# Optimization experiments

Hardware: AMD Instinct MI355X
Metric: run time of the kernel (lower is better)

## Reference

```python
import jax, jax.numpy as jnp
import numpy as np

IN_DIM = 5
HIDDEN = 256
NUM_LAYERS = 2
OUT_DIM = 3
B, T = 256, 512


def setup_inputs() -> dict:
    key = jax.random.key(0)
    ks = jax.random.split(key, 16)
    s = 1.0 / np.sqrt(HIDDEN)  # PyTorch LSTM init scale
    inp = {
        "x": jax.random.normal(ks[0], (B, T, IN_DIM), dtype=jnp.float32),
        # layer 0 (input dim 5)
        "Wih0": jax.random.uniform(ks[1], (4 * HIDDEN, IN_DIM), minval=-s, maxval=s),
        "Whh0": jax.random.uniform(ks[2], (4 * HIDDEN, HIDDEN), minval=-s, maxval=s),
        "bih0": jax.random.uniform(ks[3], (4 * HIDDEN,), minval=-s, maxval=s),
        "bhh0": jax.random.uniform(ks[4], (4 * HIDDEN,), minval=-s, maxval=s),
        # layer 1 (input dim HIDDEN)
        "Wih1": jax.random.uniform(ks[5], (4 * HIDDEN, HIDDEN), minval=-s, maxval=s),
        "Whh1": jax.random.uniform(ks[6], (4 * HIDDEN, HIDDEN), minval=-s, maxval=s),
        "bih1": jax.random.uniform(ks[7], (4 * HIDDEN,), minval=-s, maxval=s),
        "bhh1": jax.random.uniform(ks[8], (4 * HIDDEN,), minval=-s, maxval=s),
        # head: Linear(HIDDEN, 3)
        "Wh": jax.random.uniform(ks[9], (OUT_DIM, HIDDEN), minval=-s, maxval=s),
        "bh": jax.random.uniform(ks[10], (OUT_DIM,), minval=-s, maxval=s),
    }
    return inp


def _lstm_layer(x, Wih, Whh, bih, bhh):
    # x: [B, T, D_in] -> h_seq: [B, T, H]
    Bn, Tn, _ = x.shape
    H = Whh.shape[1]
    # precompute input contribution for all timesteps: [T, B, 4H]
    pre = jnp.einsum("btd,gd->tbg", x, Wih) + bih + bhh

    def step(carry, gates_in):
        h, c = carry
        gates = gates_in + h @ Whh.T  # [B, 4H]
        i, f, g, o = jnp.split(gates, 4, axis=-1)  # PyTorch gate order
        i = jax.nn.sigmoid(i)
        f = jax.nn.sigmoid(f)
        g = jnp.tanh(g)
        o = jax.nn.sigmoid(o)
        c = f * c + i * g
        h = o * jnp.tanh(c)
        return (h, c), h

    h0 = jnp.zeros((Bn, H), dtype=x.dtype)
    c0 = jnp.zeros((Bn, H), dtype=x.dtype)
    _, h_seq = jax.lax.scan(step, (h0, c0), pre)  # h_seq: [T, B, H]
    return jnp.transpose(h_seq, (1, 0, 2))  # [B, T, H]


def reference(x, Wih0, Whh0, bih0, bhh0, Wih1, Whh1, bih1, bhh1, Wh, bh):
    h = _lstm_layer(x, Wih0, Whh0, bih0, bhh0)
    h = _lstm_layer(h, Wih1, Whh1, bih1, bhh1)
    # head applied pointwise; only the last timestep is kept, so apply to last step
    last = h[:, -1, :]  # [B, H]
    y = jax.nn.sigmoid(jax.nn.relu(last) @ Wh.T + bh)  # [B, 3]
    return y[:, None, :]  # [B, 1, 3]
```

## Files before the change

### kernel.cpp

```cpp
#include <hip/hip_runtime.h>
#include <hip/hip_bf16.h>

typedef unsigned short u16;
typedef signed char i8;
typedef __attribute__((ext_vector_type(4))) float f32x4;
typedef __attribute__((ext_vector_type(4))) int i32x4;
typedef __attribute__((ext_vector_type(8))) short bf16x8;
typedef __attribute__((ext_vector_type(2))) unsigned int u32x2;

#define HID 256
#define NG 1024
#define TSTEPS 512
#define BATCH 256
#define CH 16
#define NCH 32
#define BB 4
#define HSTR 288
#define LOG2E 1.4426950408889634f
#define PRE_TSTR 262144
#define H0C_TSTR 65536

#define GB0 128
#define GB1 160
#define NBLK 224

#define MFMA_BF16(a, b, c) __builtin_amdgcn_mfma_f32_16x16x32_bf16((a), (b), (c), 0, 0, 0)
#define MFMA_I8(a, b, c)   __builtin_amdgcn_mfma_i32_16x16x64_i8((a), (b), (c), 0, 0, 0)

__device__ __forceinline__ float rcpf_(float x) {
#if __has_builtin(__builtin_amdgcn_rcpf)
    return __builtin_amdgcn_rcpf(x);
#else
    return 1.f / x;
#endif
}
__device__ __forceinline__ float exp2_(float x) {
#if __has_builtin(__builtin_amdgcn_exp2f)
    return __builtin_amdgcn_exp2f(x);
#else
    return exp2f(x);
#endif
}
__device__ __forceinline__ float sigm2(float y) { return rcpf_(1.f + exp2_(-y)); }
__device__ __forceinline__ float tanh2(float y2) { return fmaf(-2.f, rcpf_(exp2_(y2) + 1.f), 1.f); }
__device__ __forceinline__ u16 f2bf(float v){ __hip_bfloat16 h=__float2bfloat16(v); return __builtin_bit_cast(u16,h); }
__device__ __forceinline__ float bf2f(u16 u){ unsigned x=((unsigned)u)<<16; return __builtin_bit_cast(float,x); }

__global__ void prep_a(const float* __restrict__ Whh0, const float* __restrict__ Whh1,
                       const float* __restrict__ bih0, const float* __restrict__ bhh0,
                       const float* __restrict__ bih1, const float* __restrict__ bhh1,
                       float* __restrict__ qs0, float* __restrict__ dq0s,
                       float* __restrict__ qs1, float* __restrict__ dq1s,
                       float* __restrict__ b0s, float* __restrict__ b1s) {
    int r = blockIdx.x * blockDim.x + threadIdx.x;
    if (r >= NG) return;
    float m0 = 1e-20f, m1 = 1e-20f;
    for (int k = 0; k < HID; k++) {
        m0 = fmaxf(m0, fabsf(Whh0[r * HID + k]));
        m1 = fmaxf(m1, fabsf(Whh1[r * HID + k]));
    }
    qs0[r] = 127.f / m0;   dq0s[r] = m0 / 16129.f * LOG2E;
    qs1[r] = 127.f / m1;   dq1s[r] = m1 / 16129.f * LOG2E;
    b0s[r] = (bih0[r] + bhh0[r]) * LOG2E;
    b1s[r] = (bih1[r] + bhh1[r]) * LOG2E;
}

__global__ void prep_b(const float* __restrict__ x,
    const float* __restrict__ Wih0, const float* __restrict__ Whh0,
    const float* __restrict__ Wih1, const float* __restrict__ Whh1,
    const float* __restrict__ qs0, const float* __restrict__ qs1,
    i8* __restrict__ wi80, i8* __restrict__ wi81,
    u16* __restrict__ wih1f, u16* __restrict__ wih0f,
    i8* __restrict__ hs0, i8* __restrict__ hs1,
    float* __restrict__ cs0, float* __restrict__ cs1, u16* __restrict__ xpad)
{
    const int stride = gridDim.x * blockDim.x;
    const int tid = blockIdx.x * blockDim.x + threadIdx.x;
    for (int i = tid; i < NG * HID; i += stride) {
        int e = i & 15, l = (i >> 4) & 63, kc = (i >> 10) & 3, gt = i >> 12;
        int row = 16 * gt + (l & 15);
        int k = kc * 64 + (l >> 4) * 16 + e;
        float q0 = __builtin_rintf(Whh0[row * HID + k] * qs0[row]);
        float q1 = __builtin_rintf(Whh1[row * HID + k] * qs1[row]);
        wi80[i] = (i8)fminf(fmaxf(q0, -127.f), 127.f);
        wi81[i] = (i8)fminf(fmaxf(q1, -127.f), 127.f);
    }
    for (int i = tid; i < NG * HID; i += stride) {
        int gt = i >> 12, kk = (i >> 9) & 7, l = (i >> 3) & 63, e = i & 7;
        wih1f[i] = f2bf(Wih1[(16 * gt + (l & 15)) * HID + kk * 32 + (l >> 4) * 8 + e] * LOG2E);
    }
    for (int i = tid; i < 32768; i += stride) {
        int gt = i >> 9, l = (i >> 3) & 63, e = i & 7;
        int k = (l >> 4) * 8 + e;
        wih0f[i] = (k < 5) ? f2bf(Wih0[(16 * gt + (l & 15)) * 5 + k] * LOG2E) : (u16)0;
    }
    for (int i = tid; i < TSTEPS * BATCH * 8; i += stride) {
        int tok = i >> 3, k = i & 7, t = tok >> 8, b = tok & 255;
        xpad[i] = (k < 5) ? f2bf(x[((size_t)b * TSTEPS + t) * 5 + k]) : (u16)0;
    }
    for (int i = tid; i < BATCH * HID; i += stride) { hs0[i] = 0; hs1[i] = 0; cs0[i] = 0.f; cs1[i] = 0.f; }
}

__global__ __launch_bounds__(1024) __attribute__((amdgpu_waves_per_eu(4, 4)))
void stage_fused(int L,
    const u16* __restrict__ xpad8, const u16* __restrict__ wih0f, const float* __restrict__ b0s,
    const u16* __restrict__ wih1f, const float* __restrict__ b1s,
    u16* __restrict__ p0w, const u16* __restrict__ p0r,
    u16* __restrict__ h0w, const u16* __restrict__ h0r,
    u16* __restrict__ p1w, const u16* __restrict__ p1r,
    const i8* __restrict__ wi80, const i8* __restrict__ wi81,
    const float* __restrict__ dq0s, const float* __restrict__ dq1s,
    i8* __restrict__ hs0, i8* __restrict__ hs1,
    float* __restrict__ cs0, float* __restrict__ cs1)
{
    __shared__ __align__(16) char smem[16384];
    const int bid = blockIdx.x;
    const int tid = threadIdx.x, lane = tid & 63;
    const int col = lane & 15, kgrp = lane >> 4;

    if (bid < GB0) {
        const int layer = bid >> 6;
        if (layer == 0) { if (L < 1 || L > NCH) return; }
        else            { if (L < 3 || L > NCH + 2) return; }
        i8 (*h_lds)[BB * HSTR] = (i8 (*)[BB * HSTR])smem;
        const int btile = bid & 63;
        const u16* pre   = layer ? p1r : p0r;
        const i8*  wi8   = layer ? wi81 : wi80;
        const float* dq  = layer ? dq1s : dq0s;
        i8*    h_state   = layer ? hs1 : hs0;
        float* c_state   = layer ? cs1 : cs0;
        const int w = tid >> 6;
        const int b0 = btile * BB;
        const int u = w * 16 + col;

        float sc[4];
        i32x4 wv[4][4];
#pragma unroll
        for (int j = 0; j < 4; j++) {
            const int gt = 16 * j + w;
            sc[j] = dq[gt * 16 + col];
#pragma unroll
            for (int kc = 0; kc < 4; kc++)
                wv[j][kc] = ((const i32x4*)wi8)[(gt * 4 + kc) * 64 + lane];
        }
        if (tid < 64 * BB) {
            const int rrow = tid >> 6, cc = (tid & 63) * 4;
            *(int*)&h_lds[0][rrow * HSTR + cc] = *(const int*)&h_state[(b0 + rrow) * HID + cc];
        }
        float c_reg = c_state[(size_t)(b0 + kgrp) * HID + u];

        const u16* pb = pre + ((size_t)btile << 12) + (u << 2) + kgrp;
        u16 pvA[4], pvB[4];
#pragma unroll
        for (int j = 0; j < 4; j++) pvA[j] = pb[j << 10];
        const size_t h0base = ((((size_t)(w >> 1) * 16 + (btile >> 2)) * 4
                               + ((w & 1) * 2 + (col >> 3))) * 16
                              + ((btile & 3) * 4 + kgrp)) * 8 + (col & 7);
        __syncthreads();

#define REC_STEP(T, CUR, PVC, PVN) do {                                             \
        _Pragma("unroll")                                                           \
        for (int j = 0; j < 4; j++)                                                 \
            asm volatile("" : "+v"(wv[j][0]), "+v"(wv[j][1]),                       \
                              "+v"(wv[j][2]), "+v"(wv[j][3]));                      \
        i32x4 acc[4];                                                               \
        _Pragma("unroll")                                                           \
        for (int j = 0; j < 4; j++) acc[j] = (i32x4){0, 0, 0, 0};                   \
        _Pragma("unroll")                                                           \
        for (int kc = 0; kc < 4; kc++) {                                            \
            i32x4 a_ = *(const i32x4*)&h_lds[CUR][(col >> 2) * HSTR + kc * 64 + kgrp * 16]; \
            _Pragma("unroll")                                                       \
            for (int j = 0; j < 4; j++) acc[j] = MFMA_I8(a_, wv[j][kc], acc[j]);    \
        }                                                                           \
        const int tn_ = ((T) + 1 < CH) ? (T) + 1 : (T);                             \
        _Pragma("unroll")                                                           \
        for (int j = 0; j < 4; j++) PVN[j] = pb[(size_t)tn_ * PRE_TSTR + (j << 10)];\
        const float yi = fmaf((float)acc[0][0], sc[0], bf2f(PVC[0]));               \
        const float yf = fmaf((float)acc[1][0], sc[1], bf2f(PVC[1]));               \
        const float yg = fmaf((float)acc[2][0], sc[2], bf2f(PVC[2]));               \
        const float yo = fmaf((float)acc[3][0], sc[3], bf2f(PVC[3]));               \
        const float iv = sigm2(yi), fv = sigm2(yf), ov = sigm2(yo);                 \
        const float gv = tanh2(yg + yg);                                            \
        const float cn = fmaf(fv, c_reg, iv * gv);                                  \
        c_reg = cn;                                                                 \
        const float hv = ov * tanh2(cn * (2.f * LOG2E));                            \
        h_lds[(CUR) ^ 1][kgrp * HSTR + u] = (i8)__float2int_rn(hv * 127.f);         \
        if (layer == 0)                                                             \
            h0w[h0base + (size_t)(T) * H0C_TSTR] = f2bf(hv);                        \
        asm volatile("s_waitcnt lgkmcnt(0)" ::: "memory");                          \
        __builtin_amdgcn_s_barrier();                                               \
        __builtin_amdgcn_sched_barrier(0);                                          \
    } while (0)

#pragma unroll 1
        for (int t2 = 0; t2 < CH; t2 += 2) {
            REC_STEP(t2,     0, pvA, pvB);
            REC_STEP(t2 + 1, 1, pvB, pvA);
        }
#undef REC_STEP

        c_state[(size_t)(b0 + kgrp) * HID + u] = c_reg;
        if (tid < 64 * BB) {
            const int rrow = tid >> 6, cc = (tid & 63) * 4;
            *(int*)&h_state[(b0 + rrow) * HID + cc] = *(const int*)&h_lds[0][rrow * HSTR + cc];
        }
        return;
    } else if (bid < GB1) {
        if (L >= NCH) return;
        const int g = bid - GB0;
        const int tp = g >> 1, bh = g & 1;
        const int w = tid >> 6;
        const int j = w >> 2;
        float bias[4];
        bf16x8 wv4[4];
#pragma unroll
        for (int tm = 0; tm < 4; tm++) {
            const int tile = w * 4 + tm;
            bias[tm] = b0s[tile * 16 + col];
            wv4[tm] = *(const bf16x8*)&wih0f[((size_t)tile * 64 + lane) * 8];
        }
        const u16* Ab = xpad8 + ((size_t)L * CH + tp) * BATCH * 8;
#pragma unroll 1
        for (int bt = 0; bt < 8; bt++) {
            const int btg = bh * 8 + bt;
            bf16x8 af = {0, 0, 0, 0, 0, 0, 0, 0};
            if (kgrp == 0) af = *(const bf16x8*)&Ab[(btg * 16 + col) * 8];
            f32x4 acc[4];
#pragma unroll
            for (int tm = 0; tm < 4; tm++) acc[tm] = (f32x4){bias[tm], bias[tm], bias[tm], bias[tm]};
#pragma unroll
            for (int tm = 0; tm < 4; tm++) acc[tm] = MFMA_BF16(af, wv4[tm], acc[tm]);
#pragma unroll
            for (int tm = 0; tm < 4; tm++) {
                const int ul = ((w & 3) * 4 + tm) * 16 + col;
                const size_t off = ((((size_t)tp * 64 + btg * 4 + kgrp) * 4 + j) << 10) + (ul << 2);
                u32x2 pk;
                pk.x = (unsigned)f2bf(acc[tm][0]) | ((unsigned)f2bf(acc[tm][1]) << 16);
                pk.y = (unsigned)f2bf(acc[tm][2]) | ((unsigned)f2bf(acc[tm][3]) << 16);
                *(u32x2*)&p0w[off] = pk;
            }
        }
        return;
    } else {
        if (L < 2 || L > NCH + 1) return;
        const int g = bid - GB1;
        const int tp = g >> 2, j = g & 3;
        const int w = tid >> 6;
        const int gt = j * 16 + w;
        const float bias = b1s[gt * 16 + col];
        bf16x8 wv8[8];
#pragma unroll
        for (int kk = 0; kk < 8; kk++)
            wv8[kk] = *(const bf16x8*)&wih1f[((size_t)(gt * 8 + kk) * 64 + lane) * 8];
        u16* As = (u16*)smem;
        const u16* Asrc = h0r + (size_t)tp * H0C_TSTR;
        const int kks = tid >> 7;
        const int e4 = (tid & 127) * 4;
        {
            u32x2 st = *(const u32x2*)&Asrc[((size_t)kks * 16 + 0) * 512 + e4];
            *(u32x2*)&As[kks * 512 + e4] = st;
        }
        __syncthreads();
#pragma unroll 1
        for (int bt = 0; bt < 16; bt++) {
            const int cur = bt & 1, nxt = cur ^ 1;
            u32x2 nx;
            if (bt + 1 < 16)
                nx = *(const u32x2*)&Asrc[((size_t)kks * 16 + bt + 1) * 512 + e4];
            bf16x8 a8[8];
#pragma unroll
            for (int kk = 0; kk < 8; kk++)
                a8[kk] = *(const bf16x8*)&As[cur * 4096 + kk * 512 + lane * 8];
            f32x4 acc = (f32x4){bias, bias, bias, bias};
#pragma unroll
            for (int kk = 0; kk < 8; kk++)
                acc = MFMA_BF16(a8[kk], wv8[kk], acc);
            const int ul = w * 16 + col;
            const size_t off = ((((size_t)tp * 64 + bt * 4 + kgrp) * 4 + j) << 10) + (ul << 2);
            u32x2 pk;
            pk.x = (unsigned)f2bf(acc[0]) | ((unsigned)f2bf(acc[1]) << 16);
            pk.y = (unsigned)f2bf(acc[2]) | ((unsigned)f2bf(acc[3]) << 16);
            *(u32x2*)&p1w[off] = pk;
            if (bt + 1 < 16)
                *(u32x2*)&As[nxt * 4096 + kks * 512 + e4] = nx;
            __syncthreads();
        }
        return;
    }
}

__global__ void head_kernel(const i8* __restrict__ hs1,
                            const float* __restrict__ Wh, const float* __restrict__ bh,
                            float* __restrict__ y) {
    int b = blockIdx.x;
    int l = threadIdx.x;
    const float inv127 = 1.f / 127.f;
    float hr[4];
#pragma unroll
    for (int i = 0; i < 4; ++i) hr[i] = fmaxf((float)hs1[b * HID + l + 64 * i] * inv127, 0.f);
    for (int o = 0; o < 3; ++o) {
        float s = 0.f;
#pragma unroll
        for (int i = 0; i < 4; ++i) s += hr[i] * Wh[o * HID + l + 64 * i];
        for (int off = 32; off > 0; off >>= 1) s += __shfl_down(s, off, 64);
        if (l == 0) y[b * 3 + o] = 1.f / (1.f + exp2_(-(s + bh[o]) * LOG2E));
    }
}

extern "C" void kernel_launch(void* const* d_in, const int* in_sizes, int n_in,
                              void* d_out, int out_size, void* d_ws, size_t ws_size,
                              hipStream_t stream) {
    const float* x    = (const float*)d_in[0];
    const float* Wih0 = (const float*)d_in[1];
    const float* Whh0 = (const float*)d_in[2];
    const float* bih0 = (const float*)d_in[3];
    const float* bhh0 = (const float*)d_in[4];
    const float* Wih1 = (const float*)d_in[5];
    const float* Whh1 = (const float*)d_in[6];
    const float* bih1 = (const float*)d_in[7];
    const float* bhh1 = (const float*)d_in[8];
    const float* Wh   = (const float*)d_in[9];
    const float* bh   = (const float*)d_in[10];

    char* ws = (char*)d_ws;
    i8*    wi80  = (i8*)(ws);
    i8*    wi81  = (i8*)(ws + ((size_t)256 << 10));
    u16*   wih1f = (u16*)(ws + ((size_t)512 << 10));
    u16*   wih0f = (u16*)(ws + ((size_t)1024 << 10));
    float* qs0   = (float*)(ws + ((size_t)1088 << 10));
    float* dq0s  = (float*)(ws + ((size_t)1092 << 10));
    float* qs1   = (float*)(ws + ((size_t)1096 << 10));
    float* dq1s  = (float*)(ws + ((size_t)1100 << 10));
    float* b0s   = (float*)(ws + ((size_t)1104 << 10));
    float* b1s   = (float*)(ws + ((size_t)1108 << 10));
    i8*    hs0   = (i8*)(ws + ((size_t)1112 << 10));
    i8*    hs1   = (i8*)(ws + ((size_t)1176 << 10));
    float* cs0   = (float*)(ws + ((size_t)1240 << 10));
    float* cs1   = (float*)(ws + ((size_t)1496 << 10));
    u16*   xpad  = (u16*)(ws + ((size_t)1752 << 10));
    u16*   h0c   = (u16*)(ws + ((size_t)3800 << 10));
    u16*   pre0  = (u16*)(ws + ((size_t)7896 << 10));
    u16*   pre1  = (u16*)(ws + ((size_t)24280 << 10));
    const size_t PRE_ELE = (size_t)CH * BATCH * NG;
    const size_t H0C_ELE = (size_t)CH * BATCH * HID;

    prep_a<<<4, 256, 0, stream>>>(Whh0, Whh1, bih0, bhh0, bih1, bhh1,
                                  qs0, dq0s, qs1, dq1s, b0s, b1s);
    prep_b<<<1024, 256, 0, stream>>>(x, Wih0, Whh0, Wih1, Whh1, qs0, qs1,
                                     wi80, wi81, wih1f, wih0f, hs0, hs1, cs0, cs1, xpad);
    for (int L = 0; L <= NCH + 2; L++) {
        const size_t pA = (size_t)(L & 1), pB = pA ^ 1;
        stage_fused<<<NBLK, 1024, 0, stream>>>(L, xpad, wih0f, b0s, wih1f, b1s,
            pre0 + pA * PRE_ELE,
            pre0 + pB * PRE_ELE,
            h0c  + pB * H0C_ELE,
            h0c  + pA * H0C_ELE,
            pre1 + pA * PRE_ELE,
            pre1 + pB * PRE_ELE,
            wi80, wi81, dq0s, dq1s, hs0, hs1, cs0, cs1);
    }
    head_kernel<<<BATCH, 64, 0, stream>>>(hs1, Wh, bh, (float*)d_out);
}
```

Measured before the change: 633.8 us.

## Replace per-chunk stage launches with one persistent kernel synchronized by atomic flags

Replaces the host loop of 35 stage_fused launches with a single persistent kernel. Its producer and consumer block groups are ordered through global atomic counters with spin-waits. Recurrent h and c state stays in LDS and registers across chunks instead of being written to and reloaded from global memory at each chunk boundary. This removes launch overhead and per-launch state reloads. In exchange it depends on all 224 blocks being resident at once, and the spin-waits and release/acquire ordering could deadlock or add latency. A large dynamic LDS request is added, likely to force one block per CU.

```diff
diff --git a/kernel.cpp b/kernel.cpp
--- a/kernel.cpp
+++ b/kernel.cpp
@@ -19,10 +19,11 @@
 #define LOG2E 1.4426950408889634f
 #define PRE_TSTR 262144
 #define H0C_TSTR 65536
-
-#define GB0 128
-#define GB1 160
+#define PRE_ELE  4194304
+#define H0C_ELE  1048576
+
 #define NBLK 224
+#define DYN_LDS 86016
 
 #define MFMA_BF16(a, b, c) __builtin_amdgcn_mfma_f32_16x16x32_bf16((a), (b), (c), 0, 0, 0)
 #define MFMA_I8(a, b, c)   __builtin_amdgcn_mfma_i32_16x16x64_i8((a), (b), (c), 0, 0, 0)
@@ -71,8 +72,7 @@
     const float* __restrict__ qs0, const float* __restrict__ qs1,
     i8* __restrict__ wi80, i8* __restrict__ wi81,
     u16* __restrict__ wih1f, u16* __restrict__ wih0f,
-    i8* __restrict__ hs0, i8* __restrict__ hs1,
-    float* __restrict__ cs0, float* __restrict__ cs1, u16* __restrict__ xpad)
+    u16* __restrict__ xpad, int* __restrict__ flags)
 {
     const int stride = gridDim.x * blockDim.x;
     const int tid = blockIdx.x * blockDim.x + threadIdx.x;
@@ -98,37 +98,41 @@
         int tok = i >> 3, k = i & 7, t = tok >> 8, b = tok & 255;
         xpad[i] = (k < 5) ? f2bf(x[((size_t)b * TSTEPS + t) * 5 + k]) : (u16)0;
     }
-    for (int i = tid; i < BATCH * HID; i += stride) { hs0[i] = 0; hs1[i] = 0; cs0[i] = 0.f; cs1[i] = 0.f; }
+    for (int i = tid; i < 256; i += stride) flags[i] = 0;
 }
 
 __global__ __launch_bounds__(1024) __attribute__((amdgpu_waves_per_eu(4, 4)))
-void stage_fused(int L,
+void persistent_fused(
     const u16* __restrict__ xpad8, const u16* __restrict__ wih0f, const float* __restrict__ b0s,
     const u16* __restrict__ wih1f, const float* __restrict__ b1s,
-    u16* __restrict__ p0w, const u16* __restrict__ p0r,
-    u16* __restrict__ h0w, const u16* __restrict__ h0r,
-    u16* __restrict__ p1w, const u16* __restrict__ p1r,
+    u16* __restrict__ pre0, u16* __restrict__ h0c, u16* __restrict__ pre1,
     const i8* __restrict__ wi80, const i8* __restrict__ wi81,
     const float* __restrict__ dq0s, const float* __restrict__ dq1s,
-    i8* __restrict__ hs0, i8* __restrict__ hs1,
-    float* __restrict__ cs0, float* __restrict__ cs1)
+    i8* __restrict__ hs1, int* __restrict__ flags)
 {
-    __shared__ __align__(16) char smem[16384];
+    extern __shared__ __align__(16) char smem[];
     const int bid = blockIdx.x;
     const int tid = threadIdx.x, lane = tid & 63;
     const int col = lane & 15, kgrp = lane >> 4;
 
-    if (bid < GB0) {
+    int* g0c = flags;
+    int* r0c = flags + 64;
+    int* g1c = flags + 128;
+    int* r1c = flags + 192;
+
+#define SPIN_WAIT(P, TGT) do {                                                      \
+        while (__hip_atomic_load((P), __ATOMIC_RELAXED, __HIP_MEMORY_SCOPE_AGENT)   \
+               < (TGT))                                                             \
+            __builtin_amdgcn_s_sleep(2);                                            \
+        (void)__hip_atomic_load((P), __ATOMIC_ACQUIRE, __HIP_MEMORY_SCOPE_AGENT);   \
+    } while (0)
+
+    if (bid < 128) {
         const int layer = bid >> 6;
-        if (layer == 0) { if (L < 1 || L > NCH) return; }
-        else            { if (L < 3 || L > NCH + 2) return; }
+        const int btile = bid & 63;
         i8 (*h_lds)[BB * HSTR] = (i8 (*)[BB * HSTR])smem;
-        const int btile = bid & 63;
-        const u16* pre   = layer ? p1r : p0r;
         const i8*  wi8   = layer ? wi81 : wi80;
         const float* dq  = layer ? dq1s : dq0s;
-        i8*    h_state   = layer ? hs1 : hs0;
-        float* c_state   = layer ? cs1 : cs0;
         const int w = tid >> 6;
         const int b0 = btile * BB;
         const int u = w * 16 + col;
@@ -145,18 +149,32 @@
         }
         if (tid < 64 * BB) {
             const int rrow = tid >> 6, cc = (tid & 63) * 4;
-            *(int*)&h_lds[0][rrow * HSTR + cc] = *(const int*)&h_state[(b0 + rrow) * HID + cc];
-        }
-        float c_reg = c_state[(size_t)(b0 + kgrp) * HID + u];
-
-        const u16* pb = pre + ((size_t)btile << 12) + (u << 2) + kgrp;
-        u16 pvA[4], pvB[4];
-#pragma unroll
-        for (int j = 0; j < 4; j++) pvA[j] = pb[j << 10];
+            *(int*)&h_lds[0][rrow * HSTR + cc] = 0;
+        }
+        float c_reg = 0.f;
+
+        const u16* pb0 = (layer ? pre1 : pre0) + ((size_t)btile << 12) + (u << 2) + kgrp;
         const size_t h0base = ((((size_t)(w >> 1) * 16 + (btile >> 2)) * 4
                                + ((w & 1) * 2 + (col >> 3))) * 16
                               + ((btile & 3) * 4 + kgrp)) * 8 + (col & 7);
         __syncthreads();
+
+#pragma unroll 1
+        for (int c = 0; c < NCH; ++c) {
+            if (tid == 0) {
+                if (layer == 0) {
+                    SPIN_WAIT(&g0c[c], 32);
+                    if (c >= 2) SPIN_WAIT(&g1c[c - 2], 64);
+                } else {
+                    SPIN_WAIT(&g1c[c], 64);
+                }
+            }
+            __syncthreads();
+            const u16* pb = pb0 + (size_t)(c & 1) * PRE_ELE;
+            u16* h0wc = h0c + (size_t)(c & 1) * H0C_ELE;
+            u16 pvA[4], pvB[4];
+#pragma unroll
+            for (int j = 0; j < 4; j++) pvA[j] = pb[j << 10];
 
 #define REC_STEP(T, CUR, PVC, PVN) do {                                             \
         _Pragma("unroll")                                                           \
@@ -186,28 +204,31 @@
         const float hv = ov * tanh2(cn * (2.f * LOG2E));                            \
         h_lds[(CUR) ^ 1][kgrp * HSTR + u] = (i8)__float2int_rn(hv * 127.f);         \
         if (layer == 0)                                                             \
-            h0w[h0base + (size_t)(T) * H0C_TSTR] = f2bf(hv);                        \
+            h0wc[h0base + (size_t)(T) * H0C_TSTR] = f2bf(hv);                       \
         asm volatile("s_waitcnt lgkmcnt(0)" ::: "memory");                          \
         __builtin_amdgcn_s_barrier();                                               \
         __builtin_amdgcn_sched_barrier(0);                                          \
     } while (0)
 
 #pragma unroll 1
-        for (int t2 = 0; t2 < CH; t2 += 2) {
-            REC_STEP(t2,     0, pvA, pvB);
-            REC_STEP(t2 + 1, 1, pvB, pvA);
-        }
+            for (int t2 = 0; t2 < CH; t2 += 2) {
+                REC_STEP(t2,     0, pvA, pvB);
+                REC_STEP(t2 + 1, 1, pvB, pvA);
+            }
 #undef REC_STEP
 
-        c_state[(size_t)(b0 + kgrp) * HID + u] = c_reg;
-        if (tid < 64 * BB) {
+            __syncthreads();
+            if (tid == 0)
+                __hip_atomic_fetch_add(layer ? &r1c[c] : &r0c[c], 1,
+                                       __ATOMIC_RELEASE, __HIP_MEMORY_SCOPE_AGENT);
+        }
+        if (layer == 1 && tid < 64 * BB) {
             const int rrow = tid >> 6, cc = (tid & 63) * 4;
-            *(int*)&h_state[(b0 + rrow) * HID + cc] = *(const int*)&h_lds[0][rrow * HSTR + cc];
+            *(int*)&hs1[(b0 + rrow) * HID + cc] = *(const int*)&h_lds[0][rrow * HSTR + cc];
         }
         return;
-    } else if (bid < GB1) {
-        if (L >= NCH) return;
-        const int g = bid - GB0;
+    } else if (bid < 160) {
+        const int g = bid - 128;
         const int tp = g >> 1, bh = g & 1;
         const int w = tid >> 6;
         const int j = w >> 2;
@@ -219,31 +240,39 @@
             bias[tm] = b0s[tile * 16 + col];
             wv4[tm] = *(const bf16x8*)&wih0f[((size_t)tile * 64 + lane) * 8];
         }
-        const u16* Ab = xpad8 + ((size_t)L * CH + tp) * BATCH * 8;
-#pragma unroll 1
-        for (int bt = 0; bt < 8; bt++) {
-            const int btg = bh * 8 + bt;
-            bf16x8 af = {0, 0, 0, 0, 0, 0, 0, 0};
-            if (kgrp == 0) af = *(const bf16x8*)&Ab[(btg * 16 + col) * 8];
-            f32x4 acc[4];
-#pragma unroll
-            for (int tm = 0; tm < 4; tm++) acc[tm] = (f32x4){bias[tm], bias[tm], bias[tm], bias[tm]};
-#pragma unroll
-            for (int tm = 0; tm < 4; tm++) acc[tm] = MFMA_BF16(af, wv4[tm], acc[tm]);
-#pragma unroll
-            for (int tm = 0; tm < 4; tm++) {
-                const int ul = ((w & 3) * 4 + tm) * 16 + col;
-                const size_t off = ((((size_t)tp * 64 + btg * 4 + kgrp) * 4 + j) << 10) + (ul << 2);
-                u32x2 pk;
-                pk.x = (unsigned)f2bf(acc[tm][0]) | ((unsigned)f2bf(acc[tm][1]) << 16);
-                pk.y = (unsigned)f2bf(acc[tm][2]) | ((unsigned)f2bf(acc[tm][3]) << 16);
-                *(u32x2*)&p0w[off] = pk;
-            }
+#pragma unroll 1
+        for (int c = 0; c < NCH; ++c) {
+            if (tid == 0 && c >= 2) SPIN_WAIT(&r0c[c - 2], 64);
+            __syncthreads();
+            const u16* Ab = xpad8 + ((size_t)c * CH + tp) * BATCH * 8;
+            u16* p0wc = pre0 + (size_t)(c & 1) * PRE_ELE;
+#pragma unroll 1
+            for (int bt = 0; bt < 8; bt++) {
+                const int btg = bh * 8 + bt;
+                bf16x8 af = {0, 0, 0, 0, 0, 0, 0, 0};
+                if (kgrp == 0) af = *(const bf16x8*)&Ab[(btg * 16 + col) * 8];
+                f32x4 acc[4];
+#pragma unroll
+                for (int tm = 0; tm < 4; tm++) acc[tm] = (f32x4){bias[tm], bias[tm], bias[tm], bias[tm]};
+#pragma unroll
+                for (int tm = 0; tm < 4; tm++) acc[tm] = MFMA_BF16(af, wv4[tm], acc[tm]);
+#pragma unroll
+                for (int tm = 0; tm < 4; tm++) {
+                    const int ul = ((w & 3) * 4 + tm) * 16 + col;
+                    const size_t off = ((((size_t)tp * 64 + btg * 4 + kgrp) * 4 + j) << 10) + (ul << 2);
+                    u32x2 pk;
+                    pk.x = (unsigned)f2bf(acc[tm][0]) | ((unsigned)f2bf(acc[tm][1]) << 16);
+                    pk.y = (unsigned)f2bf(acc[tm][2]) | ((unsigned)f2bf(acc[tm][3]) << 16);
+                    *(u32x2*)&p0wc[off] = pk;
+                }
+            }
+            __syncthreads();
+            if (tid == 0)
+                __hip_atomic_fetch_add(&g0c[c], 1, __ATOMIC_RELEASE, __HIP_MEMORY_SCOPE_AGENT);
         }
         return;
     } else {
-        if (L < 2 || L > NCH + 1) return;
-        const int g = bid - GB1;
+        const int g = bid - 160;
         const int tp = g >> 2, j = g & 3;
         const int w = tid >> 6;
         const int gt = j * 16 + w;
@@ -253,40 +282,53 @@
         for (int kk = 0; kk < 8; kk++)
             wv8[kk] = *(const bf16x8*)&wih1f[((size_t)(gt * 8 + kk) * 64 + lane) * 8];
         u16* As = (u16*)smem;
-        const u16* Asrc = h0r + (size_t)tp * H0C_TSTR;
         const int kks = tid >> 7;
         const int e4 = (tid & 127) * 4;
-        {
-            u32x2 st = *(const u32x2*)&Asrc[((size_t)kks * 16 + 0) * 512 + e4];
-            *(u32x2*)&As[kks * 512 + e4] = st;
-        }
-        __syncthreads();
-#pragma unroll 1
-        for (int bt = 0; bt < 16; bt++) {
-            const int cur = bt & 1, nxt = cur ^ 1;
-            u32x2 nx;
-            if (bt + 1 < 16)
-                nx = *(const u32x2*)&Asrc[((size_t)kks * 16 + bt + 1) * 512 + e4];
-            bf16x8 a8[8];
-#pragma unroll
-            for (int kk = 0; kk < 8; kk++)
-                a8[kk] = *(const bf16x8*)&As[cur * 4096 + kk * 512 + lane * 8];
-            f32x4 acc = (f32x4){bias, bias, bias, bias};
-#pragma unroll
-            for (int kk = 0; kk < 8; kk++)
-                acc = MFMA_BF16(a8[kk], wv8[kk], acc);
-            const int ul = w * 16 + col;
-            const size_t off = ((((size_t)tp * 64 + bt * 4 + kgrp) * 4 + j) << 10) + (ul << 2);
-            u32x2 pk;
-            pk.x = (unsigned)f2bf(acc[0]) | ((unsigned)f2bf(acc[1]) << 16);
-            pk.y = (unsigned)f2bf(acc[2]) | ((unsigned)f2bf(acc[3]) << 16);
-            *(u32x2*)&p1w[off] = pk;
-            if (bt + 1 < 16)
-                *(u32x2*)&As[nxt * 4096 + kks * 512 + e4] = nx;
-            __syncthreads();
+#pragma unroll 1
+        for (int c = 0; c < NCH; ++c) {
+            if (tid == 0) {
+                SPIN_WAIT(&r0c[c], 64);
+                if (c >= 2) SPIN_WAIT(&r1c[c - 2], 64);
+            }
+            __syncthreads();
+            const u16* Asrc = h0c + (size_t)(c & 1) * H0C_ELE + (size_t)tp * H0C_TSTR;
+            u16* p1wc = pre1 + (size_t)(c & 1) * PRE_ELE;
+            {
+                u32x2 st = *(const u32x2*)&Asrc[((size_t)kks * 16 + 0) * 512 + e4];
+                *(u32x2*)&As[kks * 512 + e4] = st;
+            }
+            __syncthreads();
+#pragma unroll 1
+            for (int bt = 0; bt < 16; bt++) {
+                const int cur = bt & 1, nxt = cur ^ 1;
+                u32x2 nx;
+                if (bt + 1 < 16)
+                    nx = *(const u32x2*)&Asrc[((size_t)kks * 16 + bt + 1) * 512 + e4];
+                bf16x8 a8[8];
+#pragma unroll
+                for (int kk = 0; kk < 8; kk++)
+                    a8[kk] = *(const bf16x8*)&As[cur * 4096 + kk * 512 + lane * 8];
+                f32x4 acc = (f32x4){bias, bias, bias, bias};
+#pragma unroll
+                for (int kk = 0; kk < 8; kk++)
+                    acc = MFMA_BF16(a8[kk], wv8[kk], acc);
+                const int ul = w * 16 + col;
+                const size_t off = ((((size_t)tp * 64 + bt * 4 + kgrp) * 4 + j) << 10) + (ul << 2);
+                u32x2 pk;
+                pk.x = (unsigned)f2bf(acc[0]) | ((unsigned)f2bf(acc[1]) << 16);
+                pk.y = (unsigned)f2bf(acc[2]) | ((unsigned)f2bf(acc[3]) << 16);
+                *(u32x2*)&p1wc[off] = pk;
+                if (bt + 1 < 16)
+                    *(u32x2*)&As[nxt * 4096 + kks * 512 + e4] = nx;
+                __syncthreads();
+            }
+            __syncthreads();
+            if (tid == 0)
+                __hip_atomic_fetch_add(&g1c[c], 1, __ATOMIC_RELEASE, __HIP_MEMORY_SCOPE_AGENT);
         }
         return;
     }
+#undef SPIN_WAIT
 }
 
 __global__ void head_kernel(const i8* __restrict__ hs1,
@@ -333,31 +375,19 @@
     float* dq1s  = (float*)(ws + ((size_t)1100 << 10));
     float* b0s   = (float*)(ws + ((size_t)1104 << 10));
     float* b1s   = (float*)(ws + ((size_t)1108 << 10));
-    i8*    hs0   = (i8*)(ws + ((size_t)1112 << 10));
     i8*    hs1   = (i8*)(ws + ((size_t)1176 << 10));
-    float* cs0   = (float*)(ws + ((size_t)1240 << 10));
-    float* cs1   = (float*)(ws + ((size_t)1496 << 10));
+    int*   flags = (int*)(ws + ((size_t)1440 << 10));
     u16*   xpad  = (u16*)(ws + ((size_t)1752 << 10));
     u16*   h0c   = (u16*)(ws + ((size_t)3800 << 10));
     u16*   pre0  = (u16*)(ws + ((size_t)7896 << 10));
     u16*   pre1  = (u16*)(ws + ((size_t)24280 << 10));
-    const size_t PRE_ELE = (size_t)CH * BATCH * NG;
-    const size_t H0C_ELE = (size_t)CH * BATCH * HID;
 
     prep_a<<<4, 256, 0, stream>>>(Whh0, Whh1, bih0, bhh0, bih1, bhh1,
                                   qs0, dq0s, qs1, dq1s, b0s, b1s);
     prep_b<<<1024, 256, 0, stream>>>(x, Wih0, Whh0, Wih1, Whh1, qs0, qs1,
-                                     wi80, wi81, wih1f, wih0f, hs0, hs1, cs0, cs1, xpad);
-    for (int L = 0; L <= NCH + 2; L++) {
-        const size_t pA = (size_t)(L & 1), pB = pA ^ 1;
-        stage_fused<<<NBLK, 1024, 0, stream>>>(L, xpad, wih0f, b0s, wih1f, b1s,
-            pre0 + pA * PRE_ELE,
-            pre0 + pB * PRE_ELE,
-            h0c  + pB * H0C_ELE,
-            h0c  + pA * H0C_ELE,
-            pre1 + pA * PRE_ELE,
-            pre1 + pB * PRE_ELE,
-            wi80, wi81, dq0s, dq1s, hs0, hs1, cs0, cs1);
-    }
+                                     wi80, wi81, wih1f, wih0f, xpad, flags);
+    persistent_fused<<<NBLK, 1024, DYN_LDS, stream>>>(
+        xpad, wih0f, b0s, wih1f, b1s, pre0, h0c, pre1,
+        wi80, wi81, dq0s, dq1s, hs1, flags);
     head_kernel<<<BATCH, 64, 0, stream>>>(hs1, Wh, bh, (float*)d_out);
 }
```

Result: slower. 858.4 us (+35.4%).
